# Optimization experiments

Measured on AMD Instinct MI355X. Metric: run time of the kernel, lower is better.

## Reference

```python
import jax, jax.numpy as jnp
import numpy as np

D = 1024       # latent_size
LW = 16        # leaf_width
DEPTH = 8      # tree depth
NN = 2**DEPTH - 1   # internal decision nodes
NL = 2**DEPTH       # leaves
B, S = 2, 1024


def _fff(x, nw, nb, w1, b1, w2, b2, act):
    """Hard-routed Fast FeedForward (eval mode).
    x: (B,S,D); nw: (NN,D); nb: (NN,); w1: (NL,D,LW); b1: (NL,LW);
    w2: (NL,LW,D); b2: (NL,D).
    """
    node = jnp.zeros(x.shape[:2], dtype=jnp.int32)
    for _ in range(DEPTH):
        logit = jnp.einsum('bsd,bsd->bs', x, nw[node]) + nb[node]
        node = 2 * node + 1 + (logit > 0).astype(jnp.int32)
    leaf = node - NN  # (B,S) in [0, NL)
    h = act(jnp.einsum('bsd,bsdl->bsl', x, w1[leaf]) + b1[leaf])
    return jnp.einsum('bsl,bsld->bsd', h, w2[leaf]) + b2[leaf]


def _forward(x,
             q_nw, q_nb, q_w1, q_b1, q_w2, q_b2,
             k_nw, k_nb, k_w1, k_b1, k_w2, k_b2,
             v_nw, v_nb, v_w1, v_b1, v_w2, v_b2,
             f_nw, f_nb, f_w1, f_b1, f_w2, f_b2):
    # manual norm (torch std is unbiased; note original divides by sqrt(std+eps))
    mu = jnp.mean(x, -1, keepdims=True)
    sd = jnp.std(x, -1, ddof=1, keepdims=True)
    xn = (x - mu) / jnp.sqrt(sd + 1e-5)
    relu = jax.nn.relu
    q = _fff(xn, q_nw, q_nb, q_w1, q_b1, q_w2, q_b2, relu)
    k = _fff(xn, k_nw, k_nb, k_w1, k_b1, k_w2, k_b2, relu)
    v = _fff(xn, v_nw, v_nb, v_w1, v_b1, v_w2, v_b2, relu)
    att = jax.nn.softmax(jnp.einsum('bqd,bkd->bqk', q, k) / jnp.sqrt(jnp.float32(D)), axis=-1)
    y = xn + jnp.einsum('bqk,bkd->bqd', att, v)
    gelu = lambda t: jax.nn.gelu(t, approximate=False)
    return y + _fff(y, f_nw, f_nb, f_w1, f_b1, f_w2, f_b2, gelu)


def _make_fff_params(key, scale_in, scale_leaf):
    ks = jax.random.split(key, 4)
    nw = jax.random.normal(ks[0], (NN, D), jnp.float32) * scale_in
    nb = jnp.zeros((NN,), jnp.float32)
    w1 = jax.random.normal(ks[1], (NL, D, LW), jnp.float32) * scale_in
    b1 = jax.random.normal(ks[2], (NL, LW), jnp.float32) * 0.01
    w2 = jax.random.normal(ks[3], (NL, LW, D), jnp.float32) * scale_leaf
    b2 = jnp.zeros((NL, D), jnp.float32)
    return nw, nb, w1, b1, w2, b2


def setup_inputs() -> dict:
    key = jax.random.key(0)
    kx, kq, kk, kv, kf = jax.random.split(key, 5)
    s_in = 1.0 / np.sqrt(D)
    s_lf = 1.0 / np.sqrt(LW)
    inp = {"x": jax.random.normal(kx, (B, S, D), jnp.float32)}
    for name, kk_ in (("q", kq), ("k", kk), ("v", kv), ("f", kf)):
        nw, nb, w1, b1, w2, b2 = _make_fff_params(kk_, s_in, s_lf)
        inp.update({f"{name}_nw": nw, f"{name}_nb": nb, f"{name}_w1": w1,
                    f"{name}_b1": b1, f"{name}_w2": w2, f"{name}_b2": b2})
    return inp


def reference(x,
              q_nw, q_nb, q_w1, q_b1, q_w2, q_b2,
              k_nw, k_nb, k_w1, k_b1, k_w2, k_b2,
              v_nw, v_nb, v_w1, v_b1, v_w2, v_b2,
              f_nw, f_nb, f_w1, f_b1, f_w2, f_b2):
    return _forward(x,
                    q_nw, q_nb, q_w1, q_b1, q_w2, q_b2,
                    k_nw, k_nb, k_w1, k_b1, k_w2, k_b2,
                    v_nw, v_nb, v_w1, v_b1, v_w2, v_b2,
                    f_nw, f_nb, f_w1, f_b1, f_w2, f_b2)
```

## Files before the change

kernel.cpp:

```cpp
#include <hip/hip_runtime.h>
#include <hip/hip_bf16.h>
#include <math.h>

#define DD 1024
#define LWW 16
#define NNODES 255
#define NLEAF 256
#define BB 2
#define SS 1024
#define NTOK (BB*SS)
#define PLANE ((size_t)NTOK * DD)
#define MS ((size_t)1024 * 1024)
#define MAXCHUNK 512
#define CH 8

typedef short bf16x8 __attribute__((ext_vector_type(8)));
typedef float f32x4 __attribute__((ext_vector_type(4)));

#define GLOBAL_AS __attribute__((address_space(1)))
#define LDS_AS __attribute__((address_space(3)))

__device__ __forceinline__ void gld_lds16(const void* g, void* l) {
  __builtin_amdgcn_global_load_lds((const GLOBAL_AS unsigned int*)g,
                                   (LDS_AS unsigned int*)l, 16, 0, 0);
}

__device__ __forceinline__ unsigned short f2bf(float f) {
  union { float f; unsigned int u; } v; v.f = f;
  unsigned int u = v.u;
  unsigned int lsb = (u >> 16) & 1u;
  u += 0x7fffu + lsb;
  return (unsigned short)(u >> 16);
}
__device__ __forceinline__ float bf2f(unsigned short h) {
  union { unsigned int u; float f; } v; v.u = ((unsigned int)h) << 16;
  return v.f;
}
__device__ __forceinline__ void split3(float a, unsigned short& h0,
                                       unsigned short& h1, unsigned short& h2) {
  h0 = f2bf(a);
  float r = a - bf2f(h0);
  h1 = f2bf(r);
  float r2 = r - bf2f(h1);
  h2 = f2bf(r2);
}

__global__ __launch_bounds__(256) void norm_route_kernel(
    const float* __restrict__ x, float* __restrict__ xn,
    const float* nw0, const float* nb0,
    const float* nw1, const float* nb1,
    const float* nw2, const float* nb2,
    int* __restrict__ leaf_arr, int* __restrict__ hist) {
  int tok = blockIdx.x, tid = threadIdx.x;
  int wid = tid >> 6, lane = tid & 63;
  __shared__ double rs[4], rs2[4];
  __shared__ float stats[2];
  __shared__ float xs[1024];
  const float4 v = ((const float4*)(x + (size_t)tok * DD))[tid];
  double s = (double)v.x + (double)v.y + (double)v.z + (double)v.w;
  double s2 = (double)v.x * v.x + (double)v.y * v.y + (double)v.z * v.z + (double)v.w * v.w;
  for (int o = 32; o; o >>= 1) { s += __shfl_down(s, o); s2 += __shfl_down(s2, o); }
  if (lane == 0) { rs[wid] = s; rs2[wid] = s2; }
  __syncthreads();
  if (tid == 0) {
    double ts = rs[0] + rs[1] + rs[2] + rs[3];
    double ts2 = rs2[0] + rs2[1] + rs2[2] + rs2[3];
    double mu = ts / DD;
    double var = (ts2 - DD * mu * mu) / (DD - 1);
    if (var < 0) var = 0;
    double sd = sqrt(var);
    stats[0] = (float)mu;
    stats[1] = (float)(1.0 / sqrt(sd + 1e-5));
  }
  __syncthreads();
  float mu = stats[0], inv = stats[1];
  float4 o;
  o.x = (v.x - mu) * inv; o.y = (v.y - mu) * inv;
  o.z = (v.z - mu) * inv; o.w = (v.w - mu) * inv;
  ((float4*)(xn + (size_t)tok * DD))[tid] = o;
  *(float4*)&xs[tid * 4] = o;
  __syncthreads();

  if (wid < 3) {
    const float* nws[3] = {nw0, nw1, nw2};
    const float* nbs[3] = {nb0, nb1, nb2};
    const float* nw = nws[wid];
    const float* nb = nbs[wid];
    f32x4 xq[4];
#pragma unroll
    for (int j = 0; j < 4; ++j) xq[j] = *(const f32x4*)&xs[(lane + 64 * j) * 4];
    int node = 0;
#pragma unroll 1
    for (int step = 0; step < 8; ++step) {
      const f32x4* wb = (const f32x4*)(nw + (size_t)node * DD);
      double p = 0.0;
#pragma unroll
      for (int j = 0; j < 4; ++j) {
        f32x4 w = wb[lane + 64 * j];
        p += (double)xq[j][0] * w[0] + (double)xq[j][1] * w[1] +
             (double)xq[j][2] * w[2] + (double)xq[j][3] * w[3];
      }
#pragma unroll
      for (int o2 = 1; o2 < 64; o2 <<= 1) p += __shfl_xor(p, o2);
      double logit = p + (double)nb[node];
      node = 2 * node + 1 + (logit > 0.0 ? 1 : 0);
    }
    if (lane == 0) {
      int leaf = node - NNODES;
      leaf_arr[(size_t)wid * NTOK + tok] = leaf;
      atomicAdd(&hist[wid * NLEAF + leaf], 1);
    }
  }
}

__global__ __launch_bounds__(256) void route_kernel(
    const float* __restrict__ xin,
    const float* nw0, const float* nb0,
    const float* nw1, const float* nb1,
    const float* nw2, const float* nb2,
    int* __restrict__ leaf_arr, int* __restrict__ hist, int ntree) {
  int tid = threadIdx.x, lane = tid & 63, wid = tid >> 6;
  int gw = blockIdx.x * 4 + wid;
  int tok = gw / ntree, tr = gw - tok * ntree;
  if (tok >= NTOK) return;
  const float* nws[3] = {nw0, nw1, nw2};
  const float* nbs[3] = {nb0, nb1, nb2};
  const float* nw = nws[tr];
  const float* nb = nbs[tr];
  f32x4 xq[4];
  const f32x4* xb = (const f32x4*)(xin + (size_t)tok * DD);
#pragma unroll
  for (int j = 0; j < 4; ++j) xq[j] = xb[lane + 64 * j];
  int node = 0;
#pragma unroll 1
  for (int step = 0; step < 8; ++step) {
    const f32x4* wb = (const f32x4*)(nw + (size_t)node * DD);
    double p = 0.0;
#pragma unroll
    for (int j = 0; j < 4; ++j) {
      f32x4 w = wb[lane + 64 * j];
      p += (double)xq[j][0] * w[0] + (double)xq[j][1] * w[1] +
           (double)xq[j][2] * w[2] + (double)xq[j][3] * w[3];
    }
#pragma unroll
    for (int o = 1; o < 64; o <<= 1) p += __shfl_xor(p, o);
    double logit = p + (double)nb[node];
    node = 2 * node + 1 + (logit > 0.0 ? 1 : 0);
  }
  if (lane == 0) {
    int leaf = node - NNODES;
    leaf_arr[(size_t)tr * NTOK + tok] = leaf;
    atomicAdd(&hist[tr * NLEAF + leaf], 1);
  }
}

__global__ __launch_bounds__(256) void scan_scatter_kernel(
    const int* __restrict__ hist, const int* __restrict__ leaf_arr,
    int* __restrict__ list, int4* __restrict__ desc,
    int ntree, int tree0) {
  __shared__ int buf[256];
  __shared__ int cur[256];
  __shared__ int dcnt;
  int tid = threadIdx.x;
  for (int tr = 0; tr < ntree; ++tr) {
    int slot = tree0 + tr;
    int v = hist[slot * NLEAF + tid];
    buf[tid] = v;
    if (tid == 0) dcnt = 0;
    __syncthreads();
    int run = v;
    for (int off = 1; off < 256; off <<= 1) {
      int add = (tid >= off) ? buf[tid - off] : 0;
      __syncthreads();
      run += add;
      buf[tid] = run;
      __syncthreads();
    }
    cur[tid] = run - v;
    if (v > 0) {
      int k = (v + CH - 1) / CH;
      int base = atomicAdd(&dcnt, k);
      int lo = run - v;
      for (int j = 0; j < k; ++j) {
        int s = lo + j * CH;
        int e = min(run, s + CH);
        desc[slot * MAXCHUNK + base + j] = make_int4(tid, s, e, 0);
      }
    }
    __syncthreads();
    for (int i = dcnt + tid; i < MAXCHUNK; i += 256)
      desc[slot * MAXCHUNK + i] = make_int4(-1, 0, 0, 0);
    for (int base = 0; base < NTOK; base += 256) {
      int tok = base + tid;
      int leaf = leaf_arr[(size_t)slot * NTOK + tok];
      int pos = atomicAdd(&cur[leaf], 1);
      list[(size_t)slot * NTOK + pos] = tok;
    }
    __syncthreads();
  }
}

struct LeafW {
  const float* w1[3]; const float* b1[3]; const float* w2[3]; const float* b2[3];
  unsigned short* outs[3];
  float* out_res;
};

__global__ __launch_bounds__(256) void leafmlp_kernel(
    const float* __restrict__ xin,
    const int* __restrict__ list, const int4* __restrict__ desc,
    LeafW W, int tree0, int act) {
  int ty = blockIdx.y;
  int slot = tree0 + ty;
  int4 dsc = desc[slot * MAXCHUNK + blockIdx.x];
  int leaf = dsc.x;
  if (leaf < 0) return;
  int lo = dsc.y, hi = dsc.z;
  const int* L = list + (size_t)slot * NTOK;
  const float* W1 = W.w1[ty] + (size_t)leaf * DD * LWW;
  const float* B1 = W.b1[ty] + (size_t)leaf * LWW;
  const float* W2 = W.w2[ty] + (size_t)leaf * LWW * DD;
  const float* B2 = W.b2[ty] + (size_t)leaf * DD;
  unsigned short* osp = W.outs[ty];
  int tid = threadIdx.x;
  int lane = tid & 63, wid = tid >> 6;

  __shared__ float xsl[CH][1024];
  __shared__ float hpart[4][CH][20];
  __shared__ float hs[CH][16];

  float b1c = B1[tid & 15];

  int r = tid >> 2;
  const float* W1p = W1 + (size_t)r * 16 + (tid & 3) * 4;
  f32x4 wreg[16];
#pragma unroll
  for (int p = 0; p < 16; ++p) wreg[p] = *(const f32x4*)(W1p + (size_t)p * 1024);

  int toks[CH];
#pragma unroll
  for (int t = 0; t < CH; ++t) {
    int idx = lo + t;
    toks[t] = (idx < hi) ? L[idx] : -1;
    if (toks[t] >= 0) {
      float4 v = ((const float4*)(xin + (size_t)toks[t] * DD))[tid];
      *(float4*)&xsl[t][tid * 4] = v;
    } else {
      float4 z = {0.f, 0.f, 0.f, 0.f};
      *(float4*)&xsl[t][tid * 4] = z;
    }
  }
  __syncthreads();

  f32x4 part4[CH];
#pragma unroll
  for (int t = 0; t < CH; ++t) part4[t] = (f32x4){0.f, 0.f, 0.f, 0.f};
#pragma unroll
  for (int p = 0; p < 16; ++p) {
#pragma unroll
    for (int t = 0; t < CH; ++t) {
      float xv = xsl[t][p * 64 + r];
      part4[t] += xv * wreg[p];
    }
  }

  const float* W2p = W2 + tid * 4;
  f32x4 w2a[8];
#pragma unroll
  for (int l = 0; l < 8; ++l) w2a[l] = *(const f32x4*)(W2p + (size_t)l * 1024);
  f32x4 b2v = *(const f32x4*)(B2 + tid * 4);

#pragma unroll
  for (int t = 0; t < CH; ++t) {
    f32x4 v = part4[t];
#pragma unroll
    for (int o = 4; o < 64; o <<= 1) {
      v[0] += __shfl_xor(v[0], o);
      v[1] += __shfl_xor(v[1], o);
      v[2] += __shfl_xor(v[2], o);
      v[3] += __shfl_xor(v[3], o);
    }
    if (lane < 4) *(f32x4*)&hpart[wid][t][lane * 4] = v;
  }
  __syncthreads();

  if (tid < 16 * CH) {
    int t = tid >> 4, c = tid & 15;
    float h = b1c + hpart[0][t][c] + hpart[1][t][c] + hpart[2][t][c] + hpart[3][t][c];
    if (act == 0) h = fmaxf(h, 0.f);
    else h = 0.5f * h * (1.f + erff(h * 0.70710678118654752f));
    hs[t][c] = h;
  }
  __syncthreads();

  f32x4 w2b[8];
#pragma unroll
  for (int l = 0; l < 8; ++l) w2b[l] = *(const f32x4*)(W2p + (size_t)(8 + l) * 1024);
  f32x4 acc[CH];
#pragma unroll
  for (int t = 0; t < CH; ++t) acc[t] = b2v;
#pragma unroll
  for (int l = 0; l < 8; ++l) {
#pragma unroll
    for (int t = 0; t < CH; ++t) acc[t] += w2a[l] * hs[t][l];
  }
#pragma unroll
  for (int l = 0; l < 8; ++l) {
#pragma unroll
    for (int t = 0; t < CH; ++t) acc[t] += w2b[l] * hs[t][8 + l];
  }

#pragma unroll
  for (int t = 0; t < CH; ++t) {
    if (toks[t] < 0) break;
    size_t off = (size_t)toks[t] * DD + tid * 4;
    if (osp) {
      ushort4 o0, o1, o2;
      split3(acc[t][0], o0.x, o1.x, o2.x);
      split3(acc[t][1], o0.y, o1.y, o2.y);
      split3(acc[t][2], o0.z, o1.z, o2.z);
      split3(acc[t][3], o0.w, o1.w, o2.w);
      *(ushort4*)(osp + off) = o0;
      *(ushort4*)(osp + PLANE + off) = o1;
      *(ushort4*)(osp + 2 * PLANE + off) = o2;
    } else {
      float4 xr = *(const float4*)&xsl[t][tid * 4];
      float4 o;
      o.x = xr.x + acc[t][0];
      o.y = xr.y + acc[t][1];
      o.z = xr.z + acc[t][2];
      o.w = xr.w + acc[t][3];
      *(float4*)(W.out_res + off) = o;
    }
  }
}

__global__ __launch_bounds__(256) void transpose_v(const unsigned short* __restrict__ v,
                                                   unsigned short* __restrict__ vt) {
  __shared__ unsigned short t[32][34];
  int b = blockIdx.z & 1, p = blockIdx.z >> 1;
  int s0 = blockIdx.x * 32, d0 = blockIdx.y * 32;
  int tx = threadIdx.x, ty = threadIdx.y;
  const unsigned short* vb = v + p * PLANE + (size_t)b * SS * DD;
  unsigned short* vtb = vt + p * PLANE + (size_t)b * DD * SS;
#pragma unroll
  for (int k = 0; k < 4; ++k) {
    int r = ty + 8 * k;
    t[r][tx] = vb[(size_t)(s0 + r) * DD + d0 + tx];
  }
  __syncthreads();
#pragma unroll
  for (int k = 0; k < 4; ++k) {
    int r = ty + 8 * k;
    vtb[(size_t)(d0 + r) * SS + s0 + tx] = t[tx][r];
  }
}

#define BKK 64
__global__ __launch_bounds__(256) void gemm_nt3(
    const unsigned short* __restrict__ A,
    const unsigned short* __restrict__ Bt,
    float* __restrict__ C,
    const float* __restrict__ addsrc,
    float scale) {
  __shared__ short As[3][64 * BKK];
  __shared__ short Bs[3][64 * BKK];
  int b = blockIdx.z;
  int m0 = blockIdx.x * 64, n0 = blockIdx.y * 64;
  int tid = threadIdx.x, lane = tid & 63, wid = tid >> 6;
  int wm = wid >> 1, wn = wid & 1;
  f32x4 acc[2][2] = {};

  int sk0 = (((lane & 7) ^ (lane >> 3)) * 8);
  int srow0 = wid * 8 + (lane >> 3);
  int fr = lane & 15;
  int r7 = fr & 7;

  const unsigned short* Ap[3];
  const unsigned short* Bp[3];
#pragma unroll
  for (int p = 0; p < 3; ++p) {
    Ap[p] = A + p * PLANE + b * MS;
    Bp[p] = Bt + p * PLANE + b * MS;
  }

  for (int kt = 0; kt < 1024 / BKK; ++kt) {
    int kbase = kt * BKK;
#pragma unroll
    for (int p = 0; p < 3; ++p) {
#pragma unroll
      for (int r = 0; r < 2; ++r) {
        int row = r * 32 + srow0;
        gld_lds16(Ap[p] + (size_t)(m0 + row) * 1024 + kbase + sk0, &As[p][(r * 32 + wid * 8) * BKK]);
        gld_lds16(Bp[p] + (size_t)(n0 + row) * 1024 + kbase + sk0, &Bs[p][(r * 32 + wid * 8) * BKK]);
      }
    }
    __syncthreads();
#pragma unroll
    for (int kk = 0; kk < 2; ++kk) {
      int fkc = (((kk * 4 + (lane >> 4)) ^ r7) * 8);
      bf16x8 af[3][2], bfr[3][2];
#pragma unroll
      for (int p = 0; p < 3; ++p) {
        af[p][0]  = *(const bf16x8*)&As[p][(wm * 32 + fr) * BKK + fkc];
        af[p][1]  = *(const bf16x8*)&As[p][(wm * 32 + 16 + fr) * BKK + fkc];
        bfr[p][0] = *(const bf16x8*)&Bs[p][(wn * 32 + fr) * BKK + fkc];
        bfr[p][1] = *(const bf16x8*)&Bs[p][(wn * 32 + 16 + fr) * BKK + fkc];
      }
#pragma unroll
      for (int mi = 0; mi < 2; ++mi)
#pragma unroll
        for (int ni = 0; ni < 2; ++ni) {
          acc[mi][ni] = __builtin_amdgcn_mfma_f32_16x16x32_bf16(af[2][mi], bfr[0][ni], acc[mi][ni], 0, 0, 0);
          acc[mi][ni] = __builtin_amdgcn_mfma_f32_16x16x32_bf16(af[1][mi], bfr[1][ni], acc[mi][ni], 0, 0, 0);
          acc[mi][ni] = __builtin_amdgcn_mfma_f32_16x16x32_bf16(af[0][mi], bfr[2][ni], acc[mi][ni], 0, 0, 0);
          acc[mi][ni] = __builtin_amdgcn_mfma_f32_16x16x32_bf16(af[1][mi], bfr[0][ni], acc[mi][ni], 0, 0, 0);
          acc[mi][ni] = __builtin_amdgcn_mfma_f32_16x16x32_bf16(af[0][mi], bfr[1][ni], acc[mi][ni], 0, 0, 0);
          acc[mi][ni] = __builtin_amdgcn_mfma_f32_16x16x32_bf16(af[0][mi], bfr[0][ni], acc[mi][ni], 0, 0, 0);
        }
    }
    __syncthreads();
  }

  float* Cb = C + b * MS;
  const float* Rb = addsrc ? addsrc + b * MS : nullptr;
  int crow0 = (lane >> 4) * 4, ccol = lane & 15;
#pragma unroll
  for (int mi = 0; mi < 2; ++mi)
#pragma unroll
    for (int ni = 0; ni < 2; ++ni) {
      int colg = n0 + wn * 32 + ni * 16 + ccol;
#pragma unroll
      for (int j = 0; j < 4; ++j) {
        int rowg = m0 + wm * 32 + mi * 16 + crow0 + j;
        float vv = acc[mi][ni][j] * scale;
        if (Rb) vv += Rb[(size_t)rowg * 1024 + colg];
        Cb[(size_t)rowg * 1024 + colg] = vv;
      }
    }
}

__global__ __launch_bounds__(256) void gemm_nt3_ks(
    const unsigned short* __restrict__ A,
    const unsigned short* __restrict__ Bt,
    float* __restrict__ C,
    float scale) {
  __shared__ short As[3][64 * BKK];
  __shared__ short Bs[3][64 * BKK];
  int b = blockIdx.z & 1, kh = blockIdx.z >> 1;
  int m0 = blockIdx.x * 64, n0 = blockIdx.y * 64;
  int tid = threadIdx.x, lane = tid & 63, wid = tid >> 6;
  int wm = wid >> 1, wn = wid & 1;
  f32x4 acc[2][2] = {};

  int sk0 = (((lane & 7) ^ (lane >> 3)) * 8);
  int srow0 = wid * 8 + (lane >> 3);
  int fr = lane & 15;
  int r7 = fr & 7;

  const unsigned short* Ap[3];
  const unsigned short* Bp[3];
#pragma unroll
  for (int p = 0; p < 3; ++p) {
    Ap[p] = A + p * PLANE + b * MS;
    Bp[p] = Bt + p * PLANE + b * MS;
  }

  for (int kt = kh * 8; kt < kh * 8 + 8; ++kt) {
    int kbase = kt * BKK;
#pragma unroll
    for (int p = 0; p < 3; ++p) {
#pragma unroll
      for (int r = 0; r < 2; ++r) {
        int row = r * 32 + srow0;
        gld_lds16(Ap[p] + (size_t)(m0 + row) * 1024 + kbase + sk0, &As[p][(r * 32 + wid * 8) * BKK]);
        gld_lds16(Bp[p] + (size_t)(n0 + row) * 1024 + kbase + sk0, &Bs[p][(r * 32 + wid * 8) * BKK]);
      }
    }
    __syncthreads();
#pragma unroll
    for (int kk = 0; kk < 2; ++kk) {
      int fkc = (((kk * 4 + (lane >> 4)) ^ r7) * 8);
      bf16x8 af[3][2], bfr[3][2];
#pragma unroll
      for (int p = 0; p < 3; ++p) {
        af[p][0]  = *(const bf16x8*)&As[p][(wm * 32 + fr) * BKK + fkc];
        af[p][1]  = *(const bf16x8*)&As[p][(wm * 32 + 16 + fr) * BKK + fkc];
        bfr[p][0] = *(const bf16x8*)&Bs[p][(wn * 32 + fr) * BKK + fkc];
        bfr[p][1] = *(const bf16x8*)&Bs[p][(wn * 32 + 16 + fr) * BKK + fkc];
      }
#pragma unroll
      for (int mi = 0; mi < 2; ++mi)
#pragma unroll
        for (int ni = 0; ni < 2; ++ni) {
          acc[mi][ni] = __builtin_amdgcn_mfma_f32_16x16x32_bf16(af[2][mi], bfr[0][ni], acc[mi][ni], 0, 0, 0);
          acc[mi][ni] = __builtin_amdgcn_mfma_f32_16x16x32_bf16(af[1][mi], bfr[1][ni], acc[mi][ni], 0, 0, 0);
          acc[mi][ni] = __builtin_amdgcn_mfma_f32_16x16x32_bf16(af[0][mi], bfr[2][ni], acc[mi][ni], 0, 0, 0);
          acc[mi][ni] = __builtin_amdgcn_mfma_f32_16x16x32_bf16(af[1][mi], bfr[0][ni], acc[mi][ni], 0, 0, 0);
          acc[mi][ni] = __builtin_amdgcn_mfma_f32_16x16x32_bf16(af[0][mi], bfr[1][ni], acc[mi][ni], 0, 0, 0);
          acc[mi][ni] = __builtin_amdgcn_mfma_f32_16x16x32_bf16(af[0][mi], bfr[0][ni], acc[mi][ni], 0, 0, 0);
        }
    }
    __syncthreads();
  }

  float* Cb = C + b * MS;
  int crow0 = (lane >> 4) * 4, ccol = lane & 15;
#pragma unroll
  for (int mi = 0; mi < 2; ++mi)
#pragma unroll
    for (int ni = 0; ni < 2; ++ni) {
      int colg = n0 + wn * 32 + ni * 16 + ccol;
#pragma unroll
      for (int j = 0; j < 4; ++j) {
        int rowg = m0 + wm * 32 + mi * 16 + crow0 + j;
        float vv = acc[mi][ni][j] * scale;
        __hip_atomic_fetch_add(&Cb[(size_t)rowg * 1024 + colg], vv,
                               __ATOMIC_RELAXED, __HIP_MEMORY_SCOPE_AGENT);
      }
    }
}

__global__ __launch_bounds__(256) void softmax_kernel(const float* __restrict__ sc,
                                                      unsigned short* __restrict__ P) {
  int row = blockIdx.x, tid = threadIdx.x;
  int wid = tid >> 6, lane = tid & 63;
  const float4 v = ((const float4*)(sc + (size_t)row * SS))[tid];
  float mx = fmaxf(fmaxf(v.x, v.y), fmaxf(v.z, v.w));
  for (int o = 32; o; o >>= 1) mx = fmaxf(mx, __shfl_down(mx, o));
  __shared__ float red[4];
  __shared__ float bres[2];
  if (lane == 0) red[wid] = mx;
  __syncthreads();
  if (tid == 0) bres[0] = fmaxf(fmaxf(red[0], red[1]), fmaxf(red[2], red[3]));
  __syncthreads();
  float m = bres[0];
  float e0 = expf(v.x - m), e1 = expf(v.y - m), e2 = expf(v.z - m), e3 = expf(v.w - m);
  float s = e0 + e1 + e2 + e3;
  for (int o = 32; o; o >>= 1) s += __shfl_down(s, o);
  if (lane == 0) red[wid] = s;
  __syncthreads();
  if (tid == 0) bres[1] = red[0] + red[1] + red[2] + red[3];
  __syncthreads();
  float inv = 1.f / bres[1];
  float p0 = e0 * inv, p1 = e1 * inv, p2 = e2 * inv, p3 = e3 * inv;
  ushort4 o0, o1, o2;
  split3(p0, o0.x, o1.x, o2.x);
  split3(p1, o0.y, o1.y, o2.y);
  split3(p2, o0.z, o1.z, o2.z);
  split3(p3, o0.w, o1.w, o2.w);
  size_t off = (size_t)row * SS + tid * 4;
  *(ushort4*)(P + off) = o0;
  *(ushort4*)(P + PLANE + off) = o1;
  *(ushort4*)(P + 2 * PLANE + off) = o2;
}

extern "C" void kernel_launch(void* const* d_in, const int* in_sizes, int n_in,
                              void* d_out, int out_size, void* d_ws, size_t ws_size,
                              hipStream_t stream) {
  const float* x = (const float*)d_in[0];
  const float* qp[6]; const float* kp[6]; const float* vp[6]; const float* fp[6];
  for (int i = 0; i < 6; ++i) {
    qp[i] = (const float*)d_in[1 + i];
    kp[i] = (const float*)d_in[7 + i];
    vp[i] = (const float*)d_in[13 + i];
    fp[i] = (const float*)d_in[19 + i];
  }
  char* ws = (char*)d_ws;
  float* xn           = (float*)(ws);
  unsigned short* qb  = (unsigned short*)(ws + ( 8 << 20));
  unsigned short* kb  = (unsigned short*)(ws + (20 << 20));
  unsigned short* vs  = (unsigned short*)(ws + (32 << 20));
  unsigned short* vt  = (unsigned short*)(ws + (44 << 20));
  float* sc           = (float*)(ws + (32 << 20));
  unsigned short* P   = (unsigned short*)(ws + ( 8 << 20));
  float* y            = (float*)(ws + (20 << 20));
  int* meta           = (int*)(ws + (56 << 20));
  int* hist           = meta;
  int* leaf_arr       = meta + 4096;
  int* list           = meta + 12288;
  int4* desc          = (int4*)(meta + 20480);
  float* out          = (float*)d_out;

  hipMemsetAsync(hist, 0, 1024 * sizeof(int), stream);
  norm_route_kernel<<<NTOK, 256, 0, stream>>>(x, xn, qp[0], qp[1], kp[0], kp[1], vp[0], vp[1],
                                              leaf_arr, hist);
  scan_scatter_kernel<<<1, 256, 0, stream>>>(hist, leaf_arr, list, desc, 3, 0);

  LeafW Wqkv;
  Wqkv.w1[0] = qp[2]; Wqkv.b1[0] = qp[3]; Wqkv.w2[0] = qp[4]; Wqkv.b2[0] = qp[5];
  Wqkv.w1[1] = kp[2]; Wqkv.b1[1] = kp[3]; Wqkv.w2[1] = kp[4]; Wqkv.b2[1] = kp[5];
  Wqkv.w1[2] = vp[2]; Wqkv.b1[2] = vp[3]; Wqkv.w2[2] = vp[4]; Wqkv.b2[2] = vp[5];
  Wqkv.outs[0] = qb; Wqkv.outs[1] = kb; Wqkv.outs[2] = vs;
  Wqkv.out_res = nullptr;
  leafmlp_kernel<<<dim3(MAXCHUNK, 3), 256, 0, stream>>>(xn, list, desc, Wqkv, 0, 0);

  transpose_v<<<dim3(32, 32, 6), dim3(32, 8), 0, stream>>>(vs, vt);
  hipMemsetAsync(sc, 0, (size_t)2 * 1024 * 1024 * sizeof(float), stream);
  gemm_nt3_ks<<<dim3(16, 16, 4), 256, 0, stream>>>(qb, kb, sc, 0.03125f);
  softmax_kernel<<<NTOK, 256, 0, stream>>>(sc, P);
  gemm_nt3<<<dim3(16, 16, 2), 256, 0, stream>>>(P, vt, y, xn, 1.0f);

  route_kernel<<<NTOK / 4, 256, 0, stream>>>(y, fp[0], fp[1], fp[0], fp[1], fp[0], fp[1],
                                             leaf_arr + 3 * NTOK, hist + 3 * NLEAF, 1);
  scan_scatter_kernel<<<1, 256, 0, stream>>>(hist, leaf_arr, list, desc, 1, 3);

  LeafW Wf;
  Wf.w1[0] = fp[2]; Wf.b1[0] = fp[3]; Wf.w2[0] = fp[4]; Wf.b2[0] = fp[5];
  Wf.w1[1] = fp[2]; Wf.b1[1] = fp[3]; Wf.w2[1] = fp[4]; Wf.b2[1] = fp[5];
  Wf.w1[2] = fp[2]; Wf.b1[2] = fp[3]; Wf.w2[2] = fp[4]; Wf.b2[2] = fp[5];
  Wf.outs[0] = nullptr; Wf.outs[1] = nullptr; Wf.outs[2] = nullptr;
  Wf.out_res = out;
  leafmlp_kernel<<<dim3(MAXCHUNK, 1), 256, 0, stream>>>(y, list, desc, Wf, 3, 1);
}
```

Baseline: 194.5 us.

## Use 128x128 tiled 512-thread GEMM for attention, drop split-K atomics

Both attention GEMMs, scores and P·V, now use one kernel with 128x128 output tiles and 512 threads, so each wave computes a 32x64 sub-tile. The split-K atomic scores kernel and the memset that zeroed its output are removed. The aim is more operand reuse per LDS load and no atomic or memset traffic. The cost is a grid of only 128 blocks, fewer than the CU count, each running the full K loop, and about 96KB of LDS per block, which limits occupancy.

```diff
diff --git a/kernel.cpp b/kernel.cpp
--- a/kernel.cpp
+++ b/kernel.cpp
@@ -357,19 +357,19 @@
 }
 
 #define BKK 64
-__global__ __launch_bounds__(256) void gemm_nt3(
+__global__ __launch_bounds__(512) void gemm_nt3_big(
     const unsigned short* __restrict__ A,
     const unsigned short* __restrict__ Bt,
     float* __restrict__ C,
     const float* __restrict__ addsrc,
     float scale) {
-  __shared__ short As[3][64 * BKK];
-  __shared__ short Bs[3][64 * BKK];
+  __shared__ short As[3][128 * BKK];
+  __shared__ short Bs[3][128 * BKK];
   int b = blockIdx.z;
-  int m0 = blockIdx.x * 64, n0 = blockIdx.y * 64;
+  int m0 = blockIdx.x * 128, n0 = blockIdx.y * 128;
   int tid = threadIdx.x, lane = tid & 63, wid = tid >> 6;
   int wm = wid >> 1, wn = wid & 1;
-  f32x4 acc[2][2] = {};
+  f32x4 acc[2][4] = {};
 
   int sk0 = (((lane & 7) ^ (lane >> 3)) * 8);
   int srow0 = wid * 8 + (lane >> 3);
@@ -390,27 +390,28 @@
     for (int p = 0; p < 3; ++p) {
 #pragma unroll
       for (int r = 0; r < 2; ++r) {
-        int row = r * 32 + srow0;
-        gld_lds16(Ap[p] + (size_t)(m0 + row) * 1024 + kbase + sk0, &As[p][(r * 32 + wid * 8) * BKK]);
-        gld_lds16(Bp[p] + (size_t)(n0 + row) * 1024 + kbase + sk0, &Bs[p][(r * 32 + wid * 8) * BKK]);
+        int row = r * 64 + srow0;
+        gld_lds16(Ap[p] + (size_t)(m0 + row) * 1024 + kbase + sk0, &As[p][(r * 64 + wid * 8) * BKK]);
+        gld_lds16(Bp[p] + (size_t)(n0 + row) * 1024 + kbase + sk0, &Bs[p][(r * 64 + wid * 8) * BKK]);
       }
     }
     __syncthreads();
 #pragma unroll
     for (int kk = 0; kk < 2; ++kk) {
       int fkc = (((kk * 4 + (lane >> 4)) ^ r7) * 8);
-      bf16x8 af[3][2], bfr[3][2];
+      bf16x8 af[3][2], bfr[3][4];
 #pragma unroll
       for (int p = 0; p < 3; ++p) {
-        af[p][0]  = *(const bf16x8*)&As[p][(wm * 32 + fr) * BKK + fkc];
-        af[p][1]  = *(const bf16x8*)&As[p][(wm * 32 + 16 + fr) * BKK + fkc];
-        bfr[p][0] = *(const bf16x8*)&Bs[p][(wn * 32 + fr) * BKK + fkc];
-        bfr[p][1] = *(const bf16x8*)&Bs[p][(wn * 32 + 16 + fr) * BKK + fkc];
+        af[p][0] = *(const bf16x8*)&As[p][(wm * 32 + fr) * BKK + fkc];
+        af[p][1] = *(const bf16x8*)&As[p][(wm * 32 + 16 + fr) * BKK + fkc];
+#pragma unroll
+        for (int ni = 0; ni < 4; ++ni)
+          bfr[p][ni] = *(const bf16x8*)&Bs[p][(wn * 64 + ni * 16 + fr) * BKK + fkc];
       }
 #pragma unroll
       for (int mi = 0; mi < 2; ++mi)
 #pragma unroll
-        for (int ni = 0; ni < 2; ++ni) {
+        for (int ni = 0; ni < 4; ++ni) {
           acc[mi][ni] = __builtin_amdgcn_mfma_f32_16x16x32_bf16(af[2][mi], bfr[0][ni], acc[mi][ni], 0, 0, 0);
           acc[mi][ni] = __builtin_amdgcn_mfma_f32_16x16x32_bf16(af[1][mi], bfr[1][ni], acc[mi][ni], 0, 0, 0);
           acc[mi][ni] = __builtin_amdgcn_mfma_f32_16x16x32_bf16(af[0][mi], bfr[2][ni], acc[mi][ni], 0, 0, 0);
@@ -428,95 +429,14 @@
 #pragma unroll
   for (int mi = 0; mi < 2; ++mi)
 #pragma unroll
-    for (int ni = 0; ni < 2; ++ni) {
-      int colg = n0 + wn * 32 + ni * 16 + ccol;
+    for (int ni = 0; ni < 4; ++ni) {
+      int colg = n0 + wn * 64 + ni * 16 + ccol;
 #pragma unroll
       for (int j = 0; j < 4; ++j) {
         int rowg = m0 + wm * 32 + mi * 16 + crow0 + j;
         float vv = acc[mi][ni][j] * scale;
         if (Rb) vv += Rb[(size_t)rowg * 1024 + colg];
         Cb[(size_t)rowg * 1024 + colg] = vv;
-      }
-    }
-}
-
-__global__ __launch_bounds__(256) void gemm_nt3_ks(
-    const unsigned short* __restrict__ A,
-    const unsigned short* __restrict__ Bt,
-    float* __restrict__ C,
-    float scale) {
-  __shared__ short As[3][64 * BKK];
-  __shared__ short Bs[3][64 * BKK];
-  int b = blockIdx.z & 1, kh = blockIdx.z >> 1;
-  int m0 = blockIdx.x * 64, n0 = blockIdx.y * 64;
-  int tid = threadIdx.x, lane = tid & 63, wid = tid >> 6;
-  int wm = wid >> 1, wn = wid & 1;
-  f32x4 acc[2][2] = {};
-
-  int sk0 = (((lane & 7) ^ (lane >> 3)) * 8);
-  int srow0 = wid * 8 + (lane >> 3);
-  int fr = lane & 15;
-  int r7 = fr & 7;
-
-  const unsigned short* Ap[3];
-  const unsigned short* Bp[3];
-#pragma unroll
-  for (int p = 0; p < 3; ++p) {
-    Ap[p] = A + p * PLANE + b * MS;
-    Bp[p] = Bt + p * PLANE + b * MS;
-  }
-
-  for (int kt = kh * 8; kt < kh * 8 + 8; ++kt) {
-    int kbase = kt * BKK;
-#pragma unroll
-    for (int p = 0; p < 3; ++p) {
-#pragma unroll
-      for (int r = 0; r < 2; ++r) {
-        int row = r * 32 + srow0;
-        gld_lds16(Ap[p] + (size_t)(m0 + row) * 1024 + kbase + sk0, &As[p][(r * 32 + wid * 8) * BKK]);
-        gld_lds16(Bp[p] + (size_t)(n0 + row) * 1024 + kbase + sk0, &Bs[p][(r * 32 + wid * 8) * BKK]);
-      }
-    }
-    __syncthreads();
-#pragma unroll
-    for (int kk = 0; kk < 2; ++kk) {
-      int fkc = (((kk * 4 + (lane >> 4)) ^ r7) * 8);
-      bf16x8 af[3][2], bfr[3][2];
-#pragma unroll
-      for (int p = 0; p < 3; ++p) {
-        af[p][0]  = *(const bf16x8*)&As[p][(wm * 32 + fr) * BKK + fkc];
-        af[p][1]  = *(const bf16x8*)&As[p][(wm * 32 + 16 + fr) * BKK + fkc];
-        bfr[p][0] = *(const bf16x8*)&Bs[p][(wn * 32 + fr) * BKK + fkc];
-        bfr[p][1] = *(const bf16x8*)&Bs[p][(wn * 32 + 16 + fr) * BKK + fkc];
-      }
-#pragma unroll
-      for (int mi = 0; mi < 2; ++mi)
-#pragma unroll
-        for (int ni = 0; ni < 2; ++ni) {
-          acc[mi][ni] = __builtin_amdgcn_mfma_f32_16x16x32_bf16(af[2][mi], bfr[0][ni], acc[mi][ni], 0, 0, 0);
-          acc[mi][ni] = __builtin_amdgcn_mfma_f32_16x16x32_bf16(af[1][mi], bfr[1][ni], acc[mi][ni], 0, 0, 0);
-          acc[mi][ni] = __builtin_amdgcn_mfma_f32_16x16x32_bf16(af[0][mi], bfr[2][ni], acc[mi][ni], 0, 0, 0);
-          acc[mi][ni] = __builtin_amdgcn_mfma_f32_16x16x32_bf16(af[1][mi], bfr[0][ni], acc[mi][ni], 0, 0, 0);
-          acc[mi][ni] = __builtin_amdgcn_mfma_f32_16x16x32_bf16(af[0][mi], bfr[1][ni], acc[mi][ni], 0, 0, 0);
-          acc[mi][ni] = __builtin_amdgcn_mfma_f32_16x16x32_bf16(af[0][mi], bfr[0][ni], acc[mi][ni], 0, 0, 0);
-        }
-    }
-    __syncthreads();
-  }
-
-  float* Cb = C + b * MS;
-  int crow0 = (lane >> 4) * 4, ccol = lane & 15;
-#pragma unroll
-  for (int mi = 0; mi < 2; ++mi)
-#pragma unroll
-    for (int ni = 0; ni < 2; ++ni) {
-      int colg = n0 + wn * 32 + ni * 16 + ccol;
-#pragma unroll
-      for (int j = 0; j < 4; ++j) {
-        int rowg = m0 + wm * 32 + mi * 16 + crow0 + j;
-        float vv = acc[mi][ni][j] * scale;
-        __hip_atomic_fetch_add(&Cb[(size_t)rowg * 1024 + colg], vv,
-                               __ATOMIC_RELAXED, __HIP_MEMORY_SCOPE_AGENT);
       }
     }
 }
@@ -596,10 +516,9 @@
   leafmlp_kernel<<<dim3(MAXCHUNK, 3), 256, 0, stream>>>(xn, list, desc, Wqkv, 0, 0);
 
   transpose_v<<<dim3(32, 32, 6), dim3(32, 8), 0, stream>>>(vs, vt);
-  hipMemsetAsync(sc, 0, (size_t)2 * 1024 * 1024 * sizeof(float), stream);
-  gemm_nt3_ks<<<dim3(16, 16, 4), 256, 0, stream>>>(qb, kb, sc, 0.03125f);
+  gemm_nt3_big<<<dim3(8, 8, 2), 512, 0, stream>>>(qb, kb, sc, nullptr, 0.03125f);
   softmax_kernel<<<NTOK, 256, 0, stream>>>(sc, P);
-  gemm_nt3<<<dim3(16, 16, 2), 256, 0, stream>>>(P, vt, y, xn, 1.0f);
+  gemm_nt3_big<<<dim3(8, 8, 2), 512, 0, stream>>>(P, vt, y, xn, 1.0f);
 
   route_kernel<<<NTOK / 4, 256, 0, stream>>>(y, fp[0], fp[1], fp[0], fp[1], fp[0], fp[1],
                                              leaf_arr + 3 * NTOK, hist + 3 * NLEAF, 1);
```

Result: slower. 225.5 us (+16.0%).
